# Kernel optimization log

Hardware: AMD Instinct MI355X
Metric: run time of the kernel (lower is better)

Reference implementation:

```python
import jax, jax.numpy as jnp
import numpy as np
from jax import lax

N_KERNELS = 10000
IN_CH = 3
BATCH = 64
T_LEN = 1024
KSIZES = [7, 9, 11]
DILS = [1, 2, 4, 8, 16]
MAXK = max(KSIZES)

# Deterministic stand-in for torch's random per-kernel (size, dilation) draw.
_rng = np.random.default_rng(0)
_ks = np.array(KSIZES)[_rng.integers(0, len(KSIZES), N_KERNELS)]
_dil = np.array(DILS)[_rng.integers(0, len(DILS), N_KERNELS)]
GROUPS = []  # (kernel_size, dilation, static index array)
for _k in KSIZES:
    for _d in DILS:
        _idx = np.nonzero((_ks == _k) & (_dil == _d))[0]
        if _idx.size:
            GROUPS.append((_k, _d, _idx))
_PERM = np.concatenate([g[2] for g in GROUPS])  # grouped order -> original kernel id
INV_PERM = np.argsort(_PERM)                    # restore original kernel order


def setup_inputs() -> dict:
    key = jax.random.key(0)
    kx, kw, kb = jax.random.split(key, 3)
    x = jax.random.normal(kx, (BATCH, IN_CH, T_LEN), dtype=jnp.float32)
    # Weights padded to MAXK taps; taps beyond each kernel's size are zeroed
    # (zero taps do not change the conv output within the valid window).
    w = jax.random.normal(kw, (N_KERNELS, IN_CH, MAXK), dtype=jnp.float32)
    tap_mask = (np.arange(MAXK)[None, :] < _ks[:, None]).astype(np.float32)
    weights = w * jnp.asarray(tap_mask)[:, None, :]
    biases = 0.1 * jax.random.normal(kb, (N_KERNELS,), dtype=jnp.float32)
    return {"x": x, "weights": weights, "biases": biases}


def _rocket(x, weights, biases):
    # Group kernels by (size, dilation) -> <=15 batched convs instead of 10000 tiny ones.
    maxs, ppvs = [], []
    for k, d, idx in GROUPS:
        w = weights[idx, :, :k]                 # (G, C, k), idx is a static np array
        pad = (k - 1) * d // 2                  # 'same' padding (k odd -> exact)
        out = lax.conv_general_dilated(
            x, w, window_strides=(1,), padding=[(pad, pad)],
            rhs_dilation=(d,), dimension_numbers=("NCH", "OIH", "NCH"))
        out = out + biases[idx][None, :, None]  # (B, G, T)
        maxs.append(out.max(-1))                             # max pooling feature
        ppvs.append((out > 0).astype(jnp.float32).mean(-1))  # PPV feature
    mx = jnp.concatenate(maxs, 1)[:, INV_PERM]  # (B, N) in original kernel order
    pv = jnp.concatenate(ppvs, 1)[:, INV_PERM]
    # Interleave [max_0, ppv_0, max_1, ppv_1, ...] like torch.stack(features, dim=1)
    return jnp.stack([mx, pv], -1).reshape(x.shape[0], 2 * N_KERNELS)


def reference(x, weights, biases):
    return _rocket(x, weights, biases)
```

## Files before the change

### kernel.cpp

```cpp
#include <hip/hip_runtime.h>
#include <stdint.h>

#define N_KERNELS 10000
#define NCHUNK 56
#define CHUNK 256
#define CH_ALLOC 1312
#define PP_STRIDE (3 * CH_ALLOC)

typedef unsigned __int128 u128;
typedef __attribute__((ext_vector_type(8)))  short short8;
typedef __attribute__((ext_vector_type(16))) float floatx16;
typedef __attribute__((ext_vector_type(4)))  unsigned int uint4v;

struct KDraws { uint8_t k[N_KERNELS]; uint8_t d[N_KERNELS]; };

constexpr KDraws make_kd() {
    KDraws kd{};
    const u128 MULT = (((u128)0x2360ED051FC65DA4ULL) << 64) | 0x4385DF649FCCF645ULL;

    uint32_t hc = 0x43b0d7e5u;
    uint32_t pool[4] = {};
    for (int i = 0; i < 4; i++) {
        uint32_t v = 0u;
        v ^= hc; hc *= 0x931e8875u;
        v *= hc; v ^= v >> 16;
        pool[i] = v;
    }
    for (int s = 0; s < 4; s++)
        for (int dd = 0; dd < 4; dd++)
            if (s != dd) {
                uint32_t hv = pool[s];
                hv ^= hc; hc *= 0x931e8875u;
                hv *= hc; hv ^= hv >> 16;
                uint32_t rr = 0xca01f9ddu * pool[dd] - 0x4973f715u * hv;
                rr ^= rr >> 16;
                pool[dd] = rr;
            }
    uint32_t st[8] = {};
    uint32_t hcb = 0x8b51f9ddu;
    for (int i = 0; i < 8; i++) {
        uint32_t dv = pool[i & 3];
        dv ^= hcb; hcb *= 0x58f38dedu;
        dv *= hcb; dv ^= dv >> 16;
        st[i] = dv;
    }
    uint64_t w0 = (uint64_t)st[0] | ((uint64_t)st[1] << 32);
    uint64_t w1 = (uint64_t)st[2] | ((uint64_t)st[3] << 32);
    uint64_t w2 = (uint64_t)st[4] | ((uint64_t)st[5] << 32);
    uint64_t w3 = (uint64_t)st[6] | ((uint64_t)st[7] << 32);
    u128 initstate = (((u128)w0) << 64) | w1;
    u128 initseq   = (((u128)w2) << 64) | w3;

    u128 inc   = (initseq << 1) | 1;
    u128 state = 0;
    state = state * MULT + inc;
    state += initstate;
    state = state * MULT + inc;

    u128 s = state;
    for (int t = 0; t < 10000; ++t) {
        s = s * MULT + inc;
        uint64_t hi = (uint64_t)(s >> 64), lo = (uint64_t)s;
        unsigned rot = (unsigned)(hi >> 58);
        uint64_t v = hi ^ lo;
        uint64_t o = (v >> rot) | (v << ((64u - rot) & 63u));
        uint32_t d0 = (uint32_t)o;
        uint32_t d1 = (uint32_t)(o >> 32);
        int i0 = 2 * t, i1 = 2 * t + 1;
        if (i0 < 10000) kd.k[i0] = (uint8_t)(((uint64_t)d0 * 3u) >> 32);
        else            kd.d[i0 - 10000] = (uint8_t)(((uint64_t)d0 * 5u) >> 32);
        if (i1 < 10000) kd.k[i1] = (uint8_t)(((uint64_t)d1 * 3u) >> 32);
        else            kd.d[i1 - 10000] = (uint8_t)(((uint64_t)d1 * 5u) >> 32);
    }
    return kd;
}

constexpr KDraws kdr = make_kd();

struct Tables {
    alignas(16) int sched[4 * NCHUNK];
    int list[N_KERNELS];
};

constexpr Tables make_tables(const KDraws& kd) {
    Tables T{};
    int cnt[15] = {}, off[15] = {}, cur[15] = {};
    for (int i = 0; i < 10000; ++i) cnt[(int)kd.k[i] * 5 + (int)kd.d[i]]++;
    int o = 0;
    for (int g = 0; g < 15; ++g) { off[g] = o; cur[g] = o; o += cnt[g]; }
    for (int i = 0; i < 10000; ++i) {
        int g = (int)kd.k[i] * 5 + (int)kd.d[i];
        T.list[cur[g]++] = i;
    }
    const int kv[3] = {7, 9, 11};
    int ci = 0;
    for (int g = 0; g < 15; ++g) {
        int sz = cnt[g];
        for (int s2 = 0; s2 < sz; s2 += CHUNK) {
            T.sched[4 * ci + 0] = kv[g / 5];
            T.sched[4 * ci + 1] = g % 5;
            T.sched[4 * ci + 2] = off[g] + s2;
            T.sched[4 * ci + 3] = (sz - s2 < CHUNK) ? (sz - s2) : CHUNK;
            ci++;
        }
    }
    for (; ci < NCHUNK; ci++) {
        T.sched[4 * ci + 0] = 0; T.sched[4 * ci + 1] = 0;
        T.sched[4 * ci + 2] = 0; T.sched[4 * ci + 3] = 0;
    }
    return T;
}

__constant__ Tables g_T = make_tables(kdr);

constexpr int count_chunks() {
    int cnt[15] = {};
    for (int i = 0; i < 10000; ++i) cnt[(int)kdr.k[i] * 5 + (int)kdr.d[i]]++;
    int ci = 0;
    for (int g = 0; g < 15; ++g)
        for (int s2 = 0; s2 < cnt[g]; s2 += CHUNK) ci++;
    return ci;
}
constexpr int NCHUNK_REAL = count_chunks();

__device__ __forceinline__ uint16_t f32_to_bf16(float v) {
    uint32_t u = __builtin_bit_cast(uint32_t, v);
    return (uint16_t)((u + 0x7FFFu + ((u >> 16) & 1u)) >> 16);
}

__device__ __forceinline__ void stat16(const floatx16& C, float& mx, int& cnt) {
    float g0 = fmaxf(fmaxf(C[0],  C[1]),  C[2]);
    float g1 = fmaxf(fmaxf(C[3],  C[4]),  C[5]);
    float g2 = fmaxf(fmaxf(C[6],  C[7]),  C[8]);
    float g3 = fmaxf(fmaxf(C[9],  C[10]), C[11]);
    float g4 = fmaxf(fmaxf(C[12], C[13]), C[14]);
    float h0 = fmaxf(fmaxf(g0, g1), g2);
    float h1 = fmaxf(fmaxf(g3, g4), C[15]);
    mx = fmaxf(mx, fmaxf(h0, h1));
    #pragma unroll
    for (int i = 0; i < 16; i += 2) {
        int s0 = __builtin_bit_cast(int, C[i])     >> 31;
        int s1 = __builtin_bit_cast(int, C[i + 1]) >> 31;
        cnt += s0 + s1;
    }
}

template <int K, int D>
__device__ __forceinline__ void body(const float* __restrict__ x,
                                     const float* __restrict__ wgt,
                                     const float* __restrict__ bias,
                                     int lstart, int valid,
                                     float* __restrict__ out,
                                     short* __restrict__ xs,
                                     int b) {
    constexpr int H  = (K - 1) / 2;
    constexpr int Q  = 1024 / D;
    constexpr int LQ = (Q == 1024) ? 10 : (Q == 512) ? 9 : (Q == 256) ? 8
                     : (Q == 128) ? 7 : 6;
    constexpr int S  = Q + 16;
    constexpr int OB = 8 - H;

    const int tid   = threadIdx.x;
    const int lane  = tid & 63;
    const int wave  = tid >> 6;
    const int jbase = (lane >> 5) * 8;
    const int m31   = lane & 31;
    const bool hi   = (jbase == 8);

    {
        uint4v z = (uint4v)0u;
        uint4v* xv = reinterpret_cast<uint4v*>(xs);
        #pragma unroll
        for (int i = 0; i < 8; ++i) {
            int idx = tid + i * 256;
            if (idx < (4 * PP_STRIDE) / 8) xv[idx] = z;
        }
    }
    __syncthreads();

    for (int n = tid; n < 3072; n += 256) {
        int c    = n >> 10;
        int t    = n & 1023;
        int r    = t >> LQ;
        int q    = t & (Q - 1);
        float v  = x[((size_t)b * 3 + c) * 1024 + r + D * q];
        short hv = (short)f32_to_bf16(v);
        int P    = 8 + (r << LQ) + (r << 4) + q;
        short* sb = xs + c * CH_ALLOC;
        sb[P] = hv;
        (sb + PP_STRIDE)[P - 2]     = hv;
        (sb + 2 * PP_STRIDE)[P - 4] = hv;
        (sb + 3 * PP_STRIDE)[P - 6] = hv;
    }

    short8 whi[2][3];
    {
        int i0 = wave * 64 + m31;
        int i1 = i0 + 32;
        int n0 = g_T.list[lstart + (i0 < valid ? i0 : valid - 1)];
        int n1 = g_T.list[lstart + (i1 < valid ? i1 : valid - 1)];
        float bv0 = bias[n0], bv1 = bias[n1];
        #pragma unroll
        for (int t2 = 0; t2 < 2; ++t2) {
            int n = t2 ? n1 : n0;
            float bv = t2 ? bv1 : bv0;
            #pragma unroll
            for (int c = 0; c < 3; ++c) {
                #pragma unroll
                for (int u = 0; u < 8; ++u) {
                    int j = jbase + u;
                    float wv = (j < 11) ? wgt[n * 33 + c * 11 + j] : 0.f;
                    if (c == 2 && u == 7 && hi) wv = bv;
                    whi[t2][c][u] = (short)f32_to_bf16(wv);
                }
            }
        }
    }

    __syncthreads();

    auto rd_e = [](const short* cp) -> short8 {
        return *reinterpret_cast<const short8*>(cp);
    };
    auto rd_o = [](const short* cp) -> short8 {
        uint4v dv = __builtin_bit_cast(uint4v, *reinterpret_cast<const short8*>(cp));
        uint32_t d4 = *reinterpret_cast<const uint32_t*>(cp + 8);
        uint4v t;
        t[0] = (dv[0] >> 16) | (dv[1] << 16);
        t[1] = (dv[1] >> 16) | (dv[2] << 16);
        t[2] = (dv[2] >> 16) | (dv[3] << 16);
        t[3] = (dv[3] >> 16) | (d4    << 16);
        return __builtin_bit_cast(short8, t);
    };

    float mx0 = -3.402823466e38f, mx1 = -3.402823466e38f;
    int cnt0 = 0, cnt1 = 0;

    #pragma unroll 1
    for (int ri = 0; ri < 4; ++ri) {
        int rb, qb;
        if constexpr (D == 1)      { rb = 0;                   qb = 256 * ri + 8 * m31; }
        else if constexpr (D == 2) { rb = ri >> 1;             qb = (ri & 1) * 256 + 8 * m31; }
        else if constexpr (D == 4) { rb = ri;                  qb = 8 * m31; }
        else if constexpr (D == 8) { rb = 2 * ri + (m31 >> 4); qb = 8 * (m31 & 15); }
        else                       { rb = 4 * ri + (m31 >> 3); qb = 8 * (m31 & 7); }
        const int Abase = OB + rb * S + qb + jbase;

        #pragma unroll
        for (int p = 0; p < 8; ++p) {
            const int o8 = (OB + p) & 7;
            const int ph = o8 >> 1;
            const int L  = Abase + (p - o8);
            const short* base = xs + ph * PP_STRIDE + L;
            short8 A0, A1, A2;
            if ((o8 & 1) == 0) {
                A0 = rd_e(base);
                A1 = rd_e(base + CH_ALLOC);
                A2 = rd_e(base + 2 * CH_ALLOC);
            } else {
                A0 = rd_o(base);
                A1 = rd_o(base + CH_ALLOC);
                A2 = rd_o(base + 2 * CH_ALLOC);
            }
            A2[7] = hi ? (short)0x3F80 : A2[7];

            floatx16 C0, C1;
            C0 = __builtin_amdgcn_mfma_f32_32x32x16_bf16(A0, whi[0][0],
                                                         (floatx16)(0.0f), 0, 0, 0);
            C1 = __builtin_amdgcn_mfma_f32_32x32x16_bf16(A0, whi[1][0],
                                                         (floatx16)(0.0f), 0, 0, 0);
            C0 = __builtin_amdgcn_mfma_f32_32x32x16_bf16(A1, whi[0][1], C0, 0, 0, 0);
            C1 = __builtin_amdgcn_mfma_f32_32x32x16_bf16(A1, whi[1][1], C1, 0, 0, 0);
            C0 = __builtin_amdgcn_mfma_f32_32x32x16_bf16(A2, whi[0][2], C0, 0, 0, 0);
            C1 = __builtin_amdgcn_mfma_f32_32x32x16_bf16(A2, whi[1][2], C1, 0, 0, 0);
            stat16(C0, mx0, cnt0);
            stat16(C1, mx1, cnt1);
        }
    }

    mx0  = fmaxf(mx0, __shfl_xor(mx0, 32));
    mx1  = fmaxf(mx1, __shfl_xor(mx1, 32));
    cnt0 += __shfl_xor(cnt0, 32);
    cnt1 += __shfl_xor(cnt1, 32);

    if (lane < 32) {
        int i0 = wave * 64 + m31;
        int i1 = i0 + 32;
        int n0 = g_T.list[lstart + (i0 < valid ? i0 : valid - 1)];
        int n1 = g_T.list[lstart + (i1 < valid ? i1 : valid - 1)];
        float2* ob = reinterpret_cast<float2*>(out + (size_t)b * (2 * N_KERNELS));
        ob[n0] = make_float2(mx0, (float)(1024 + cnt0) * (1.0f / 1024.0f));
        ob[n1] = make_float2(mx1, (float)(1024 + cnt1) * (1.0f / 1024.0f));
    }
}

__global__ __launch_bounds__(256, 5)
void rocket_main(const float* __restrict__ x, const float* __restrict__ wgt,
                 const float* __restrict__ bias, float* __restrict__ out) {
    __shared__ __align__(16) short xs[4 * PP_STRIDE];
    int kc     = g_T.sched[4 * blockIdx.x + 0];
    int ld2    = g_T.sched[4 * blockIdx.x + 1];
    int lstart = g_T.sched[4 * blockIdx.x + 2];
    int valid  = g_T.sched[4 * blockIdx.x + 3];
    if (valid == 0) return;
    int b = blockIdx.y;
    switch (kc * 8 + ld2) {
        case 7*8+0:  body<7, 1 >(x, wgt, bias, lstart, valid, out, xs, b); break;
        case 7*8+1:  body<7, 2 >(x, wgt, bias, lstart, valid, out, xs, b); break;
        case 7*8+2:  body<7, 4 >(x, wgt, bias, lstart, valid, out, xs, b); break;
        case 7*8+3:  body<7, 8 >(x, wgt, bias, lstart, valid, out, xs, b); break;
        case 7*8+4:  body<7, 16>(x, wgt, bias, lstart, valid, out, xs, b); break;
        case 9*8+0:  body<9, 1 >(x, wgt, bias, lstart, valid, out, xs, b); break;
        case 9*8+1:  body<9, 2 >(x, wgt, bias, lstart, valid, out, xs, b); break;
        case 9*8+2:  body<9, 4 >(x, wgt, bias, lstart, valid, out, xs, b); break;
        case 9*8+3:  body<9, 8 >(x, wgt, bias, lstart, valid, out, xs, b); break;
        case 9*8+4:  body<9, 16>(x, wgt, bias, lstart, valid, out, xs, b); break;
        case 11*8+0: body<11,1 >(x, wgt, bias, lstart, valid, out, xs, b); break;
        case 11*8+1: body<11,2 >(x, wgt, bias, lstart, valid, out, xs, b); break;
        case 11*8+2: body<11,4 >(x, wgt, bias, lstart, valid, out, xs, b); break;
        case 11*8+3: body<11,8 >(x, wgt, bias, lstart, valid, out, xs, b); break;
        default:     body<11,16>(x, wgt, bias, lstart, valid, out, xs, b); break;
    }
}

extern "C" void kernel_launch(void* const* d_in, const int* in_sizes, int n_in,
                              void* d_out, int out_size, void* d_ws, size_t ws_size,
                              hipStream_t stream) {
    const float* x   = (const float*)d_in[0];
    const float* w   = (const float*)d_in[1];
    const float* b   = (const float*)d_in[2];
    float* out = (float*)d_out;
    (void)d_ws; (void)ws_size;

    hipLaunchKernelGGL(rocket_main, dim3(NCHUNK_REAL, 64), dim3(256), 0, stream,
                       x, w, b, out);
}
```

Baseline: 128.7 us.

## Drop four-phase shifted LDS copies; read unaligned windows via dword loads

New measurement: 486.8 us. 278% more time.

```diff
diff --git a/kernel.cpp b/kernel.cpp
--- a/kernel.cpp
+++ b/kernel.cpp
@@ -4,8 +4,7 @@
 #define N_KERNELS 10000
 #define NCHUNK 56
 #define CHUNK 256
-#define CH_ALLOC 1312
-#define PP_STRIDE (3 * CH_ALLOC)
+#define CH_ALLOC 1296
 
 typedef unsigned __int128 u128;
 typedef __attribute__((ext_vector_type(8)))  short short8;
@@ -159,6 +158,7 @@
                      : (Q == 128) ? 7 : 6;
     constexpr int S  = Q + 16;
     constexpr int OB = 8 - H;
+    constexpr int CH_DW = CH_ALLOC / 2;
 
     const int tid   = threadIdx.x;
     const int lane  = tid & 63;
@@ -171,9 +171,9 @@
         uint4v z = (uint4v)0u;
         uint4v* xv = reinterpret_cast<uint4v*>(xs);
         #pragma unroll
-        for (int i = 0; i < 8; ++i) {
+        for (int i = 0; i < 2; ++i) {
             int idx = tid + i * 256;
-            if (idx < (4 * PP_STRIDE) / 8) xv[idx] = z;
+            if (idx < (3 * CH_ALLOC) / 8) xv[idx] = z;
         }
     }
     __syncthreads();
@@ -184,13 +184,8 @@
         int r    = t >> LQ;
         int q    = t & (Q - 1);
         float v  = x[((size_t)b * 3 + c) * 1024 + r + D * q];
-        short hv = (short)f32_to_bf16(v);
         int P    = 8 + (r << LQ) + (r << 4) + q;
-        short* sb = xs + c * CH_ALLOC;
-        sb[P] = hv;
-        (sb + PP_STRIDE)[P - 2]     = hv;
-        (sb + 2 * PP_STRIDE)[P - 4] = hv;
-        (sb + 3 * PP_STRIDE)[P - 6] = hv;
+        xs[c * CH_ALLOC + P] = (short)f32_to_bf16(v);
     }
 
     short8 whi[2][3];
@@ -219,22 +214,24 @@
 
     __syncthreads();
 
-    auto rd_e = [](const short* cp) -> short8 {
-        return *reinterpret_cast<const short8*>(cp);
-    };
-    auto rd_o = [](const short* cp) -> short8 {
-        uint4v dv = __builtin_bit_cast(uint4v, *reinterpret_cast<const short8*>(cp));
-        uint32_t d4 = *reinterpret_cast<const uint32_t*>(cp + 8);
-        uint4v t;
-        t[0] = (dv[0] >> 16) | (dv[1] << 16);
-        t[1] = (dv[1] >> 16) | (dv[2] << 16);
-        t[2] = (dv[2] >> 16) | (dv[3] << 16);
-        t[3] = (dv[3] >> 16) | (d4    << 16);
+    auto rd_even = [](const uint32_t* dp) -> short8 {
+        uint4v t; t[0] = dp[0]; t[1] = dp[1]; t[2] = dp[2]; t[3] = dp[3];
         return __builtin_bit_cast(short8, t);
     };
+    auto rd_odd = [](const uint32_t* dp) -> short8 {
+        uint32_t d0 = dp[0], d1 = dp[1], d2 = dp[2], d3 = dp[3], d4 = dp[4];
+        uint4v t;
+        t[0] = (d0 >> 16) | (d1 << 16);
+        t[1] = (d1 >> 16) | (d2 << 16);
+        t[2] = (d2 >> 16) | (d3 << 16);
+        t[3] = (d3 >> 16) | (d4 << 16);
+        return __builtin_bit_cast(short8, t);
+    };
 
     float mx0 = -3.402823466e38f, mx1 = -3.402823466e38f;
     int cnt0 = 0, cnt1 = 0;
+
+    const uint32_t* xd = reinterpret_cast<const uint32_t*>(xs);
 
     #pragma unroll 1
     for (int ri = 0; ri < 4; ++ri) {
@@ -245,22 +242,23 @@
         else if constexpr (D == 8) { rb = 2 * ri + (m31 >> 4); qb = 8 * (m31 & 15); }
         else                       { rb = 4 * ri + (m31 >> 3); qb = 8 * (m31 & 7); }
         const int Abase = OB + rb * S + qb + jbase;
+        const int DWb   = Abase >> 1;
 
         #pragma unroll
         for (int p = 0; p < 8; ++p) {
-            const int o8 = (OB + p) & 7;
-            const int ph = o8 >> 1;
-            const int L  = Abase + (p - o8);
-            const short* base = xs + ph * PP_STRIDE + L;
+            const int W  = OB + p;
+            const bool odd = (W & 1) != 0;
+            const int dwo = (W >> 1) - (OB >> 1);
+            const uint32_t* dp0 = xd + DWb + dwo;
             short8 A0, A1, A2;
-            if ((o8 & 1) == 0) {
-                A0 = rd_e(base);
-                A1 = rd_e(base + CH_ALLOC);
-                A2 = rd_e(base + 2 * CH_ALLOC);
+            if (!odd) {
+                A0 = rd_even(dp0);
+                A1 = rd_even(dp0 + CH_DW);
+                A2 = rd_even(dp0 + 2 * CH_DW);
             } else {
-                A0 = rd_o(base);
-                A1 = rd_o(base + CH_ALLOC);
-                A2 = rd_o(base + 2 * CH_ALLOC);
+                A0 = rd_odd(dp0);
+                A1 = rd_odd(dp0 + CH_DW);
+                A2 = rd_odd(dp0 + 2 * CH_DW);
             }
             A2[7] = hi ? (short)0x3F80 : A2[7];
 
@@ -294,10 +292,10 @@
     }
 }
 
-__global__ __launch_bounds__(256, 5)
+__global__ __launch_bounds__(256, 6)
 void rocket_main(const float* __restrict__ x, const float* __restrict__ wgt,
                  const float* __restrict__ bias, float* __restrict__ out) {
-    __shared__ __align__(16) short xs[4 * PP_STRIDE];
+    __shared__ __align__(16) short xs[3 * CH_ALLOC];
     int kc     = g_T.sched[4 * blockIdx.x + 0];
     int ld2    = g_T.sched[4 * blockIdx.x + 1];
     int lstart = g_T.sched[4 * blockIdx.x + 2];
```
